# Performance work log

Measured on AMD Instinct MI355X. Metric: run time of the kernel, lower is better.

## Reference

```python
import jax, jax.numpy as jnp
import numpy as np

PAD = 0
N_SENSE = 5

def setup_inputs() -> dict:
    key = jax.random.key(0)
    k1, k2, k3, k4, k5 = jax.random.split(key, 5)
    mb, L, S, D, V, O = 256, 200, N_SENSE, 128, 50000, 50000
    inputs = jax.random.randint(k1, (mb, L * S), 0, V, dtype=jnp.int32).astype(jnp.int64)
    length_weights = jax.random.uniform(k2, (mb, 1, 1), dtype=jnp.float32)
    word_attn_mask = jnp.zeros((mb, L), dtype=bool)
    embedding = (jax.random.normal(k3, (V, D), dtype=jnp.float32) * 0.02).at[PAD].set(0.0)
    W_out = jax.random.normal(k4, (D, O), dtype=jnp.float32) * 0.02
    b_out = jnp.zeros((O,), dtype=jnp.float32)
    w_attn = jax.random.normal(k5, (D,), dtype=jnp.float32) * 0.02
    b_attn = jnp.zeros((), dtype=jnp.float32)
    return {"inputs": inputs, "length_weights": length_weights,
            "word_attn_mask": word_attn_mask, "embedding": embedding,
            "W_out": W_out, "b_out": b_out, "w_attn": w_attn, "b_attn": b_attn}

def reference(inputs, length_weights, word_attn_mask, embedding, W_out, b_out, w_attn, b_attn):
    S = N_SENSE
    mb, LS = inputs.shape
    L = LS // S
    D = embedding.shape[1]
    lw = length_weights[:, 0, 0]                      # [mb] per-example 1/length scalar
    embeds = embedding[inputs]                        # [mb, L*S, D]
    # global mean: sum over all sense-slots, scaled by length weight / n_sense
    gmean = embeds.sum(axis=1) * lw[:, None] / S      # [mb, D]
    # sense-level attention (softmax over n_sense per word slot)
    sense_imp = jnp.einsum('bld,bd->bl', embeds, gmean).reshape(mb, L, S)
    sense_w = jax.nn.softmax(sense_imp, axis=-1)      # [mb, L, S]
    word_mean = jnp.einsum('bls,blsd->bld', sense_w, embeds.reshape(mb, L, S, D))
    # word-level attention with pad mask
    word_imp = jnp.einsum('bld,d->bl', word_mean, w_attn) + b_attn
    word_imp = jnp.where(word_attn_mask, -jnp.inf, word_imp)
    word_w = jax.nn.softmax(word_imp, axis=-1)        # [mb, L]
    context = jnp.einsum('bl,bld->bd', word_w, word_mean)  # [mb, D]
    # similarity-based sense re-weighting
    sim = jnp.einsum('bld,bd->bl', embeds, context).reshape(mb, L, S)
    attn_w = jax.nn.softmax(sim, axis=-1).reshape(mb, LS)
    attn_w = attn_w * lw[:, None]
    attn_w = jnp.where(inputs == PAD, 0.0, attn_w)
    hidden = jnp.einsum('bl,bld->bd', attn_w, embeds)  # [mb, D]
    logits = hidden @ W_out + b_out
    return jax.nn.log_softmax(logits, axis=-1)
```

## Files before the change

### kernel.cpp

```cpp
#include <hip/hip_runtime.h>
#include <hip/hip_bf16.h>
#include <stdint.h>

#define MB 256
#define LW 200
#define NS 5
#define DD 128
#define OO 50000
#define LSTOK 1000

#define NSTRIPES 782
#define EMB_BLK 391

typedef __attribute__((ext_vector_type(8))) short bf16x8;
typedef __attribute__((ext_vector_type(4))) float f32x4;

__device__ inline unsigned short f2bf(float f){
  unsigned u = __float_as_uint(f);
  unsigned r = (u + 0x7fffu + ((u >> 16) & 1u)) >> 16;
  return (unsigned short)r;
}
__device__ inline float bf2f(unsigned short h){
  return __uint_as_float(((unsigned)h) << 16);
}
__device__ inline unsigned packbf(float a, float b){
  return (unsigned)f2bf(a) | ((unsigned)f2bf(b) << 16);
}
__device__ inline float lo16f(unsigned p){ return __uint_as_float(p << 16); }
__device__ inline float hi16f(unsigned p){ return __uint_as_float(p & 0xffff0000u); }
__device__ inline float wsum64(float v){
  #pragma unroll
  for (int o = 1; o < 64; o <<= 1) v += __shfl_xor(v, o, 64);
  return v;
}
__device__ inline float wmax64(float v){
  #pragma unroll
  for (int o = 1; o < 64; o <<= 1) v = fmaxf(v, __shfl_xor(v, o, 64));
  return v;
}
__device__ inline float dot8(uint4 r, float4 a, float4 b){
  return lo16f(r.x)*a.x + hi16f(r.x)*a.y + lo16f(r.y)*a.z + hi16f(r.y)*a.w
       + lo16f(r.z)*b.x + hi16f(r.z)*b.y + lo16f(r.w)*b.z + hi16f(r.w)*b.w;
}
__device__ inline void acc8(uint4 r, float4& x, float4& y){
  x.x += lo16f(r.x); x.y += hi16f(r.x); x.z += lo16f(r.y); x.w += hi16f(r.y);
  y.x += lo16f(r.z); y.y += hi16f(r.z); y.z += lo16f(r.w); y.w += hi16f(r.w);
}
__device__ inline void wacc8(uint4 r, float w, float4& x, float4& y){
  x.x += w*lo16f(r.x); x.y += w*hi16f(r.x); x.z += w*lo16f(r.y); x.w += w*hi16f(r.y);
  y.x += w*lo16f(r.z); y.y += w*hi16f(r.z); y.z += w*lo16f(r.w); y.w += w*hi16f(r.w);
}
__device__ inline float gsum16(float v){
  v += __shfl_xor(v, 1, 64);
  v += __shfl_xor(v, 2, 64);
  v += __shfl_xor(v, 4, 64);
  v += __shfl_xor(v, 8, 64);
  return v;
}
__device__ inline float xg(float v){
  v += __shfl_xor(v, 16, 64);
  v += __shfl_xor(v, 32, 64);
  return v;
}
__device__ inline int sniff_f(const unsigned* p, int l){
  unsigned v = p[2*l + 1];
  return (__ballot(v != 0u) == 0ull) ? 1 : 0;
}

__global__ __launch_bounds__(256) void k_prep(const float* __restrict__ W,
                                              const float* __restrict__ emb,
                                              unsigned short* __restrict__ Wt,
                                              unsigned* __restrict__ embB){
  int blk = blockIdx.x, t = threadIdx.x;
  if (blk < NSTRIPES){
    __shared__ float tile[64][129];
    long long n0 = (long long)blk * 64;
    int j = t & 63, kk = t >> 6;
    #pragma unroll
    for (int k = kk; k < 128; k += 4){
      float v = 0.f;
      if (n0 + j < OO) v = W[(long long)k*OO + n0 + j];
      tile[j][k] = v;
    }
    __syncthreads();
    #pragma unroll
    for (int c = t; c < 4096; c += 256){
      int row = c >> 6, dw = c & 63;
      if (n0 + row < OO){
        unsigned pr = packbf(tile[row][2*dw], tile[row][2*dw+1]);
        ((unsigned*)Wt)[(n0 + row)*64 + dw] = pr;
      }
    }
  } else {
    long long base = (long long)(blk - NSTRIPES) * 16384;
    for (int i = t; i < 4096; i += 256){
      long long idx = base + (long long)i*4;
      if (idx < (long long)OO*DD){
        float4 v = *(const float4*)(emb + idx);
        uint2 o; o.x = packbf(v.x, v.y); o.y = packbf(v.z, v.w);
        *(uint2*)(embB + (idx >> 1)) = o;
      }
    }
  }
}

__global__ __launch_bounds__(1024)
void k_attn(
    const int* __restrict__ in32, const float* __restrict__ lwp,
    const unsigned char* __restrict__ maskp, const unsigned* __restrict__ embB,
    const float* __restrict__ w_attn, const float* __restrict__ b_attn_p,
    unsigned short* __restrict__ hB)
{
  __shared__ float wm[LW*DD];
  __shared__ float red[16*DD];
  __shared__ int   idL[1024];
  __shared__ float gm[DD];
  __shared__ float cx[DD];
  __shared__ float waL[DD];
  __shared__ float wimp[LW];
  __shared__ float ww[LW];

  int b = blockIdx.x, t = threadIdx.x;
  int wv = t >> 6, l = t & 63;
  int g = l >> 4, q16 = l & 15;
  int G = wv*4 + g;
  int f = sniff_f((const unsigned*)in32, l);
  long long base = (long long)b * LSTOK;
  float lw = lwp[b];

  idL[t] = (t < LSTOK) ? in32[(base + t) << f] : 0;
  if (t < DD) waL[t] = w_attn[t];
  __syncthreads();

  {
    float4 s0v = {0,0,0,0}, s1v = {0,0,0,0};
    #pragma unroll 4
    for (int j = 0; j < 16; j++){
      int id = idL[G*16 + j];
      uint4 r = *(const uint4*)(embB + (long long)id*64 + (q16 << 2));
      acc8(r, s0v, s1v);
    }
    s0v.x = xg(s0v.x); s0v.y = xg(s0v.y); s0v.z = xg(s0v.z); s0v.w = xg(s0v.w);
    s1v.x = xg(s1v.x); s1v.y = xg(s1v.y); s1v.z = xg(s1v.z); s1v.w = xg(s1v.w);
    if (g == 0){
      *(float4*)&red[wv*DD + q16*8]     = s0v;
      *(float4*)&red[wv*DD + q16*8 + 4] = s1v;
    }
  }
  __syncthreads();
  if (t < DD){
    float s = 0.f;
    #pragma unroll
    for (int r = 0; r < 16; r++) s += red[r*DD + t];
    gm[t] = s * lw * 0.2f;
  }
  __syncthreads();

  {
    float4 g0v = *(const float4*)&gm[q16*8];
    float4 g1v = *(const float4*)&gm[q16*8+4];
    float4 wa0 = *(const float4*)&waL[q16*8];
    float4 wa1 = *(const float4*)&waL[q16*8+4];
    float b_attn = *b_attn_p;
    for (int w = G; w < LW; w += 64){
      int tb = w*NS;
      uint4 e0 = *(const uint4*)(embB + (long long)idL[tb  ]*64 + (q16<<2));
      uint4 e1 = *(const uint4*)(embB + (long long)idL[tb+1]*64 + (q16<<2));
      uint4 e2 = *(const uint4*)(embB + (long long)idL[tb+2]*64 + (q16<<2));
      uint4 e3 = *(const uint4*)(embB + (long long)idL[tb+3]*64 + (q16<<2));
      uint4 e4 = *(const uint4*)(embB + (long long)idL[tb+4]*64 + (q16<<2));
      float d0 = gsum16(dot8(e0, g0v, g1v));
      float d1 = gsum16(dot8(e1, g0v, g1v));
      float d2 = gsum16(dot8(e2, g0v, g1v));
      float d3 = gsum16(dot8(e3, g0v, g1v));
      float d4 = gsum16(dot8(e4, g0v, g1v));
      float mx = fmaxf(fmaxf(fmaxf(d0,d1), fmaxf(d2,d3)), d4);
      float x0 = __expf(d0-mx), x1 = __expf(d1-mx), x2 = __expf(d2-mx),
            x3 = __expf(d3-mx), x4 = __expf(d4-mx);
      float inv = 1.0f / (x0+x1+x2+x3+x4);
      float4 m0 = {0,0,0,0}, m1 = {0,0,0,0};
      wacc8(e0, x0*inv, m0, m1);
      wacc8(e1, x1*inv, m0, m1);
      wacc8(e2, x2*inv, m0, m1);
      wacc8(e3, x3*inv, m0, m1);
      wacc8(e4, x4*inv, m0, m1);
      *(float4*)&wm[w*DD + q16*8]     = m0;
      *(float4*)&wm[w*DD + q16*8 + 4] = m1;
      float wi = m0.x*wa0.x + m0.y*wa0.y + m0.z*wa0.z + m0.w*wa0.w
               + m1.x*wa1.x + m1.y*wa1.y + m1.z*wa1.z + m1.w*wa1.w;
      wi = gsum16(wi);
      if (q16 == 0)
        wimp[w] = maskp[(long long)b*LW + w] ? -INFINITY : (wi + b_attn);
    }
  }
  __syncthreads();

  if (wv == 0){
    float v[4]; float mx = -INFINITY;
    #pragma unroll
    for (int j = 0; j < 4; j++){
      int i = l + 64*j;
      v[j] = (i < LW) ? wimp[i] : -INFINITY;
      mx = fmaxf(mx, v[j]);
    }
    mx = wmax64(mx);
    float s = 0.f;
    #pragma unroll
    for (int j = 0; j < 4; j++){
      int i = l + 64*j;
      if (i < LW){ v[j] = __expf(v[j]-mx); s += v[j]; }
    }
    s = wsum64(s);
    float inv = 1.0f / s;
    #pragma unroll
    for (int j = 0; j < 4; j++){
      int i = l + 64*j;
      if (i < LW) ww[i] = v[j]*inv;
    }
  }
  __syncthreads();

  {
    int d = t & 127, r = t >> 7;
    float s = 0.f;
    for (int w = r; w < LW; w += 8) s += ww[w]*wm[w*DD + d];
    red[r*DD + d] = s;
  }
  __syncthreads();
  if (t < DD){
    float s = 0.f;
    #pragma unroll
    for (int r = 0; r < 8; r++) s += red[r*DD + t];
    cx[t] = s;
  }
  __syncthreads();

  {
    float4 c0v = *(const float4*)&cx[q16*8];
    float4 c1v = *(const float4*)&cx[q16*8+4];
    float4 h0a = {0,0,0,0}, h1a = {0,0,0,0};
    for (int w = G; w < LW; w += 64){
      int tb = w*NS;
      int i0 = idL[tb], i1 = idL[tb+1], i2 = idL[tb+2], i3 = idL[tb+3], i4 = idL[tb+4];
      uint4 e0 = *(const uint4*)(embB + (long long)i0*64 + (q16<<2));
      uint4 e1 = *(const uint4*)(embB + (long long)i1*64 + (q16<<2));
      uint4 e2 = *(const uint4*)(embB + (long long)i2*64 + (q16<<2));
      uint4 e3 = *(const uint4*)(embB + (long long)i3*64 + (q16<<2));
      uint4 e4 = *(const uint4*)(embB + (long long)i4*64 + (q16<<2));
      float d0 = gsum16(dot8(e0, c0v, c1v));
      float d1 = gsum16(dot8(e1, c0v, c1v));
      float d2 = gsum16(dot8(e2, c0v, c1v));
      float d3 = gsum16(dot8(e3, c0v, c1v));
      float d4 = gsum16(dot8(e4, c0v, c1v));
      float mx = fmaxf(fmaxf(fmaxf(d0,d1), fmaxf(d2,d3)), d4);
      float x0 = __expf(d0-mx), x1 = __expf(d1-mx), x2 = __expf(d2-mx),
            x3 = __expf(d3-mx), x4 = __expf(d4-mx);
      float inv = lw / (x0+x1+x2+x3+x4);
      wacc8(e0, (i0 == 0) ? 0.f : x0*inv, h0a, h1a);
      wacc8(e1, (i1 == 0) ? 0.f : x1*inv, h0a, h1a);
      wacc8(e2, (i2 == 0) ? 0.f : x2*inv, h0a, h1a);
      wacc8(e3, (i3 == 0) ? 0.f : x3*inv, h0a, h1a);
      wacc8(e4, (i4 == 0) ? 0.f : x4*inv, h0a, h1a);
    }
    h0a.x = xg(h0a.x); h0a.y = xg(h0a.y); h0a.z = xg(h0a.z); h0a.w = xg(h0a.w);
    h1a.x = xg(h1a.x); h1a.y = xg(h1a.y); h1a.z = xg(h1a.z); h1a.w = xg(h1a.w);
    if (g == 0){
      *(float4*)&red[wv*DD + q16*8]     = h0a;
      *(float4*)&red[wv*DD + q16*8 + 4] = h1a;
    }
  }
  __syncthreads();
  if (t < DD){
    float s = 0.f;
    #pragma unroll
    for (int r = 0; r < 16; r++) s += red[r*DD + t];
    hB[b*DD + t] = f2bf(s);
  }
}

__global__ __launch_bounds__(256) void k_gemm_stats(
    const unsigned short* __restrict__ Wt,
    const unsigned short* __restrict__ hB,
    const float* __restrict__ b_out,
    float* __restrict__ stats)
{
  __shared__ unsigned short Bs[64*128];
  int blk = blockIdx.x;
  long long n0 = (long long)blk * 64;
  int t = threadIdx.x;

  #pragma unroll
  for (int c = t; c < 1024; c += 256){
    int n = c >> 4;
    int bo = (c & 15) << 4;
    long long ng = n0 + n;
    uint4 v = {0u,0u,0u,0u};
    if (ng < OO) v = *(const uint4*)((const char*)Wt + ng*256 + bo);
    *(uint4*)((char*)Bs + n*256 + (bo ^ ((n & 7) << 4))) = v;
  }
  __syncthreads();

  int wv = t >> 6, l = t & 63;
  int lr = l & 15, lg = l >> 4;

  bf16x8 a[4][4];
  #pragma unroll
  for (int mt = 0; mt < 4; mt++)
    #pragma unroll
    for (int ks = 0; ks < 4; ks++)
      a[mt][ks] = *(const bf16x8*)(hB + (wv*64 + mt*16 + lr)*DD + ks*32 + lg*8);

  f32x4 acc[4][4];
  #pragma unroll
  for (int mt = 0; mt < 4; mt++)
    #pragma unroll
    for (int nt = 0; nt < 4; nt++)
      acc[mt][nt] = (f32x4){0.f,0.f,0.f,0.f};

  #pragma unroll
  for (int nt = 0; nt < 4; nt++)
    #pragma unroll
    for (int ks = 0; ks < 4; ks++){
      int n = nt*16 + lr;
      int kb = (ks*32 + lg*8) * 2;
      bf16x8 bfr = *(const bf16x8*)((const char*)Bs + n*256 + (kb ^ ((n & 7) << 4)));
      #pragma unroll
      for (int mt = 0; mt < 4; mt++)
        acc[mt][nt] = __builtin_amdgcn_mfma_f32_16x16x32_bf16(a[mt][ks], bfr, acc[mt][nt], 0, 0, 0);
    }

  float bv[4]; int nvalid[4];
  #pragma unroll
  for (int nt = 0; nt < 4; nt++){
    long long ng = n0 + nt*16 + lr;
    nvalid[nt] = (ng < OO);
    bv[nt] = nvalid[nt] ? b_out[ng] : 0.f;
  }
  #pragma unroll
  for (int mt = 0; mt < 4; mt++){
    #pragma unroll
    for (int j = 0; j < 4; j++){
      int m = wv*64 + mt*16 + lg*4 + j;
      float s = 0.f;
      #pragma unroll
      for (int nt = 0; nt < 4; nt++)
        s += nvalid[nt] ? __expf(acc[mt][nt][j] + bv[nt]) : 0.f;
      #pragma unroll
      for (int o = 1; o < 16; o <<= 1) s += __shfl_xor(s, o, 64);
      if (lr == 0) stats[(long long)m*NSTRIPES + blk] = s;
    }
  }
}

__global__ void k_reduce(const float* __restrict__ stats, float* __restrict__ Lrow){
  int m = blockIdx.x, l = threadIdx.x;
  float s = 0.f;
  for (int i = l; i < NSTRIPES; i += 64) s += stats[(long long)m*NSTRIPES + i];
  s = wsum64(s);
  if (l == 0) Lrow[m] = __logf(s);
}

__global__ __launch_bounds__(256) void k_gemm_out(
    const unsigned short* __restrict__ Wt,
    const unsigned short* __restrict__ hB,
    const float* __restrict__ b_out,
    const float* __restrict__ Lrow,
    float* __restrict__ out)
{
  __shared__ unsigned short Bs[64*128];
  int blk = blockIdx.x;
  long long n0 = (long long)blk * 64;
  int t = threadIdx.x;

  #pragma unroll
  for (int c = t; c < 1024; c += 256){
    int n = c >> 4;
    int bo = (c & 15) << 4;
    long long ng = n0 + n;
    uint4 v = {0u,0u,0u,0u};
    if (ng < OO) v = *(const uint4*)((const char*)Wt + ng*256 + bo);
    *(uint4*)((char*)Bs + n*256 + (bo ^ ((n & 7) << 4))) = v;
  }
  __syncthreads();

  int wv = t >> 6, l = t & 63;
  int lr = l & 15, lg = l >> 4;

  bf16x8 a[4][4];
  #pragma unroll
  for (int mt = 0; mt < 4; mt++)
    #pragma unroll
    for (int ks = 0; ks < 4; ks++)
      a[mt][ks] = *(const bf16x8*)(hB + (wv*64 + mt*16 + lr)*DD + ks*32 + lg*8);

  f32x4 acc[4][4];
  #pragma unroll
  for (int mt = 0; mt < 4; mt++)
    #pragma unroll
    for (int nt = 0; nt < 4; nt++)
      acc[mt][nt] = (f32x4){0.f,0.f,0.f,0.f};

  #pragma unroll
  for (int nt = 0; nt < 4; nt++)
    #pragma unroll
    for (int ks = 0; ks < 4; ks++){
      int n = nt*16 + lr;
      int kb = (ks*32 + lg*8) * 2;
      bf16x8 bfr = *(const bf16x8*)((const char*)Bs + n*256 + (kb ^ ((n & 7) << 4)));
      #pragma unroll
      for (int mt = 0; mt < 4; mt++)
        acc[mt][nt] = __builtin_amdgcn_mfma_f32_16x16x32_bf16(a[mt][ks], bfr, acc[mt][nt], 0, 0, 0);
    }

  float bv[4]; int nvalid[4]; long long ngl[4];
  #pragma unroll
  for (int nt = 0; nt < 4; nt++){
    long long ng = n0 + nt*16 + lr;
    ngl[nt] = ng;
    nvalid[nt] = (ng < OO);
    bv[nt] = nvalid[nt] ? b_out[ng] : 0.f;
  }
  #pragma unroll
  for (int mt = 0; mt < 4; mt++){
    #pragma unroll
    for (int j = 0; j < 4; j++){
      int m = wv*64 + mt*16 + lg*4 + j;
      float Lv = Lrow[m];
      #pragma unroll
      for (int nt = 0; nt < 4; nt++)
        if (nvalid[nt]) out[(long long)m*OO + ngl[nt]] = acc[mt][nt][j] + bv[nt] - Lv;
    }
  }
}

extern "C" void kernel_launch(void* const* d_in, const int* in_sizes, int n_in,
                              void* d_out, int out_size, void* d_ws, size_t ws_size,
                              hipStream_t stream)
{
  (void)in_sizes; (void)n_in; (void)out_size; (void)ws_size;
  const void* inputs          = d_in[0];
  const float* lw             = (const float*)d_in[1];
  const unsigned char* mask   = (const unsigned char*)d_in[2];
  const float* emb            = (const float*)d_in[3];
  const float* W              = (const float*)d_in[4];
  const float* bout           = (const float*)d_in[5];
  const float* w_attn         = (const float*)d_in[6];
  const float* b_attn         = (const float*)d_in[7];

  char* ws = (char*)d_ws;
  unsigned short* Wt   = (unsigned short*)(ws);
  unsigned* embB       = (unsigned*)(ws + 12800000);
  unsigned short* hB   = (unsigned short*)(ws + 25600000);
  float* stats         = (float*)(ws + 25665536);
  float* Lrow          = (float*)(ws + 26466304);

  const int* in32 = (const int*)inputs;

  k_prep<<<NSTRIPES + EMB_BLK, 256, 0, stream>>>(W, emb, Wt, embB);
  k_attn<<<MB, 1024, 0, stream>>>(in32, lw, mask, embB, w_attn, b_attn, hB);
  k_gemm_stats<<<NSTRIPES, 256, 0, stream>>>(Wt, hB, bout, stats);
  k_reduce<<<MB, 64, 0, stream>>>(stats, Lrow);
  k_gemm_out<<<NSTRIPES, 256, 0, stream>>>(Wt, hB, bout, Lrow, (float*)d_out);
}
```

Baseline: 99.71 us.

## Remap attention gathers to 32-lane word groups with two-word load batching

The attention kernel now assigns each word to a 32-lane group, with each lane loading 4 bf16 values (uint2) instead of 16-lane groups loading 8 (uint4). The gather loops are unrolled to issue the embedding loads for two words before computing on either, so more memory requests are in flight per wave. The aim is better latency hiding on the random embedding gathers and lower register pressure per lane. The cost is one more shuffle stage in each dot-product reduction and smaller per-lane loads.

Result: slower. 107.2 us (+7.5%).

```diff
diff --git a/kernel.cpp b/kernel.cpp
--- a/kernel.cpp
+++ b/kernel.cpp
@@ -38,33 +38,28 @@
   for (int o = 1; o < 64; o <<= 1) v = fmaxf(v, __shfl_xor(v, o, 64));
   return v;
 }
-__device__ inline float dot8(uint4 r, float4 a, float4 b){
-  return lo16f(r.x)*a.x + hi16f(r.x)*a.y + lo16f(r.y)*a.z + hi16f(r.y)*a.w
-       + lo16f(r.z)*b.x + hi16f(r.z)*b.y + lo16f(r.w)*b.z + hi16f(r.w)*b.w;
-}
-__device__ inline void acc8(uint4 r, float4& x, float4& y){
-  x.x += lo16f(r.x); x.y += hi16f(r.x); x.z += lo16f(r.y); x.w += hi16f(r.y);
-  y.x += lo16f(r.z); y.y += hi16f(r.z); y.z += lo16f(r.w); y.w += hi16f(r.w);
-}
-__device__ inline void wacc8(uint4 r, float w, float4& x, float4& y){
-  x.x += w*lo16f(r.x); x.y += w*hi16f(r.x); x.z += w*lo16f(r.y); x.w += w*hi16f(r.y);
-  y.x += w*lo16f(r.z); y.y += w*hi16f(r.z); y.z += w*lo16f(r.w); y.w += w*hi16f(r.w);
-}
-__device__ inline float gsum16(float v){
+__device__ inline float dot4u(uint2 r, float4 c){
+  return lo16f(r.x)*c.x + hi16f(r.x)*c.y + lo16f(r.y)*c.z + hi16f(r.y)*c.w;
+}
+__device__ inline float gsum32(float v){
   v += __shfl_xor(v, 1, 64);
   v += __shfl_xor(v, 2, 64);
   v += __shfl_xor(v, 4, 64);
   v += __shfl_xor(v, 8, 64);
-  return v;
-}
-__device__ inline float xg(float v){
   v += __shfl_xor(v, 16, 64);
-  v += __shfl_xor(v, 32, 64);
   return v;
 }
 __device__ inline int sniff_f(const unsigned* p, int l){
   unsigned v = p[2*l + 1];
   return (__ballot(v != 0u) == 0ull) ? 1 : 0;
+}
+
+struct W5 { uint2 e[5]; };
+__device__ inline void loadw(const unsigned* __restrict__ embB,
+                             const int* __restrict__ idL, int tb, int q, W5& w){
+  #pragma unroll
+  for (int s = 0; s < 5; s++)
+    w.e[s] = *(const uint2*)(embB + (long long)idL[tb + s]*64 + (q << 1));
 }
 
 __global__ __launch_bounds__(256) void k_prep(const float* __restrict__ W,
@@ -122,8 +117,8 @@
 
   int b = blockIdx.x, t = threadIdx.x;
   int wv = t >> 6, l = t & 63;
-  int g = l >> 4, q16 = l & 15;
-  int G = wv*4 + g;
+  int g2 = l >> 5, q = l & 31;
+  int G = wv*2 + g2;
   int f = sniff_f((const unsigned*)in32, l);
   long long base = (long long)b * LSTOK;
   float lw = lwp[b];
@@ -133,19 +128,17 @@
   __syncthreads();
 
   {
-    float4 s0v = {0,0,0,0}, s1v = {0,0,0,0};
+    float4 s = {0,0,0,0};
     #pragma unroll 4
-    for (int j = 0; j < 16; j++){
-      int id = idL[G*16 + j];
-      uint4 r = *(const uint4*)(embB + (long long)id*64 + (q16 << 2));
-      acc8(r, s0v, s1v);
-    }
-    s0v.x = xg(s0v.x); s0v.y = xg(s0v.y); s0v.z = xg(s0v.z); s0v.w = xg(s0v.w);
-    s1v.x = xg(s1v.x); s1v.y = xg(s1v.y); s1v.z = xg(s1v.z); s1v.w = xg(s1v.w);
-    if (g == 0){
-      *(float4*)&red[wv*DD + q16*8]     = s0v;
-      *(float4*)&red[wv*DD + q16*8 + 4] = s1v;
-    }
+    for (int j = 0; j < 32; j++){
+      int id = idL[G*32 + j];
+      uint2 r = *(const uint2*)(embB + (long long)id*64 + (q << 1));
+      s.x += lo16f(r.x); s.y += hi16f(r.x);
+      s.z += lo16f(r.y); s.w += hi16f(r.y);
+    }
+    s.x += __shfl_xor(s.x, 32, 64); s.y += __shfl_xor(s.y, 32, 64);
+    s.z += __shfl_xor(s.z, 32, 64); s.w += __shfl_xor(s.w, 32, 64);
+    if (g2 == 0) *(float4*)&red[wv*DD + q*4] = s;
   }
   __syncthreads();
   if (t < DD){
@@ -157,40 +150,48 @@
   __syncthreads();
 
   {
-    float4 g0v = *(const float4*)&gm[q16*8];
-    float4 g1v = *(const float4*)&gm[q16*8+4];
-    float4 wa0 = *(const float4*)&waL[q16*8];
-    float4 wa1 = *(const float4*)&waL[q16*8+4];
-    float b_attn = *b_attn_p;
-    for (int w = G; w < LW; w += 64){
-      int tb = w*NS;
-      uint4 e0 = *(const uint4*)(embB + (long long)idL[tb  ]*64 + (q16<<2));
-      uint4 e1 = *(const uint4*)(embB + (long long)idL[tb+1]*64 + (q16<<2));
-      uint4 e2 = *(const uint4*)(embB + (long long)idL[tb+2]*64 + (q16<<2));
-      uint4 e3 = *(const uint4*)(embB + (long long)idL[tb+3]*64 + (q16<<2));
-      uint4 e4 = *(const uint4*)(embB + (long long)idL[tb+4]*64 + (q16<<2));
-      float d0 = gsum16(dot8(e0, g0v, g1v));
-      float d1 = gsum16(dot8(e1, g0v, g1v));
-      float d2 = gsum16(dot8(e2, g0v, g1v));
-      float d3 = gsum16(dot8(e3, g0v, g1v));
-      float d4 = gsum16(dot8(e4, g0v, g1v));
+    float4 gv  = *(const float4*)&gm[q*4];
+    float4 wav = *(const float4*)&waL[q*4];
+    float ba = *b_attn_p;
+    const unsigned char* mrow = maskp + (long long)b*LW;
+
+    auto sense_word = [&](const W5& e, int wrd){
+      float d0 = gsum32(dot4u(e.e[0], gv));
+      float d1 = gsum32(dot4u(e.e[1], gv));
+      float d2 = gsum32(dot4u(e.e[2], gv));
+      float d3 = gsum32(dot4u(e.e[3], gv));
+      float d4 = gsum32(dot4u(e.e[4], gv));
       float mx = fmaxf(fmaxf(fmaxf(d0,d1), fmaxf(d2,d3)), d4);
       float x0 = __expf(d0-mx), x1 = __expf(d1-mx), x2 = __expf(d2-mx),
             x3 = __expf(d3-mx), x4 = __expf(d4-mx);
       float inv = 1.0f / (x0+x1+x2+x3+x4);
-      float4 m0 = {0,0,0,0}, m1 = {0,0,0,0};
-      wacc8(e0, x0*inv, m0, m1);
-      wacc8(e1, x1*inv, m0, m1);
-      wacc8(e2, x2*inv, m0, m1);
-      wacc8(e3, x3*inv, m0, m1);
-      wacc8(e4, x4*inv, m0, m1);
-      *(float4*)&wm[w*DD + q16*8]     = m0;
-      *(float4*)&wm[w*DD + q16*8 + 4] = m1;
-      float wi = m0.x*wa0.x + m0.y*wa0.y + m0.z*wa0.z + m0.w*wa0.w
-               + m1.x*wa1.x + m1.y*wa1.y + m1.z*wa1.z + m1.w*wa1.w;
-      wi = gsum16(wi);
-      if (q16 == 0)
-        wimp[w] = maskp[(long long)b*LW + w] ? -INFINITY : (wi + b_attn);
+      float4 m = {0,0,0,0};
+      float w0 = x0*inv, w1 = x1*inv, w2 = x2*inv, w3 = x3*inv, w4 = x4*inv;
+      m.x = w0*lo16f(e.e[0].x) + w1*lo16f(e.e[1].x) + w2*lo16f(e.e[2].x)
+          + w3*lo16f(e.e[3].x) + w4*lo16f(e.e[4].x);
+      m.y = w0*hi16f(e.e[0].x) + w1*hi16f(e.e[1].x) + w2*hi16f(e.e[2].x)
+          + w3*hi16f(e.e[3].x) + w4*hi16f(e.e[4].x);
+      m.z = w0*lo16f(e.e[0].y) + w1*lo16f(e.e[1].y) + w2*lo16f(e.e[2].y)
+          + w3*lo16f(e.e[3].y) + w4*lo16f(e.e[4].y);
+      m.w = w0*hi16f(e.e[0].y) + w1*hi16f(e.e[1].y) + w2*hi16f(e.e[2].y)
+          + w3*hi16f(e.e[3].y) + w4*hi16f(e.e[4].y);
+      *(float4*)&wm[wrd*DD + q*4] = m;
+      float wi = gsum32(m.x*wav.x + m.y*wav.y + m.z*wav.z + m.w*wav.w);
+      if (q == 0) wimp[wrd] = mrow[wrd] ? -INFINITY : (wi + ba);
+    };
+
+    for (int it = 0; it < 6; it += 2){
+      int wA = G + it*32, wB = wA + 32;
+      W5 eA, eB;
+      loadw(embB, idL, wA*NS, q, eA);
+      loadw(embB, idL, wB*NS, q, eB);
+      sense_word(eA, wA);
+      sense_word(eB, wB);
+    }
+    if (G < 8){
+      int wA = 192 + G;
+      W5 eA; loadw(embB, idL, wA*NS, q, eA);
+      sense_word(eA, wA);
     }
   }
   __syncthreads();
@@ -236,38 +237,51 @@
   __syncthreads();
 
   {
-    float4 c0v = *(const float4*)&cx[q16*8];
-    float4 c1v = *(const float4*)&cx[q16*8+4];
-    float4 h0a = {0,0,0,0}, h1a = {0,0,0,0};
-    for (int w = G; w < LW; w += 64){
-      int tb = w*NS;
-      int i0 = idL[tb], i1 = idL[tb+1], i2 = idL[tb+2], i3 = idL[tb+3], i4 = idL[tb+4];
-      uint4 e0 = *(const uint4*)(embB + (long long)i0*64 + (q16<<2));
-      uint4 e1 = *(const uint4*)(embB + (long long)i1*64 + (q16<<2));
-      uint4 e2 = *(const uint4*)(embB + (long long)i2*64 + (q16<<2));
-      uint4 e3 = *(const uint4*)(embB + (long long)i3*64 + (q16<<2));
-      uint4 e4 = *(const uint4*)(embB + (long long)i4*64 + (q16<<2));
-      float d0 = gsum16(dot8(e0, c0v, c1v));
-      float d1 = gsum16(dot8(e1, c0v, c1v));
-      float d2 = gsum16(dot8(e2, c0v, c1v));
-      float d3 = gsum16(dot8(e3, c0v, c1v));
-      float d4 = gsum16(dot8(e4, c0v, c1v));
+    float4 cv = *(const float4*)&cx[q*4];
+    float4 ha = {0,0,0,0};
+
+    auto sim_word = [&](const W5& e, int tb){
+      int i0 = idL[tb], i1 = idL[tb+1], i2 = idL[tb+2],
+          i3 = idL[tb+3], i4 = idL[tb+4];
+      float d0 = gsum32(dot4u(e.e[0], cv));
+      float d1 = gsum32(dot4u(e.e[1], cv));
+      float d2 = gsum32(dot4u(e.e[2], cv));
+      float d3 = gsum32(dot4u(e.e[3], cv));
+      float d4 = gsum32(dot4u(e.e[4], cv));
       float mx = fmaxf(fmaxf(fmaxf(d0,d1), fmaxf(d2,d3)), d4);
       float x0 = __expf(d0-mx), x1 = __expf(d1-mx), x2 = __expf(d2-mx),
             x3 = __expf(d3-mx), x4 = __expf(d4-mx);
       float inv = lw / (x0+x1+x2+x3+x4);
-      wacc8(e0, (i0 == 0) ? 0.f : x0*inv, h0a, h1a);
-      wacc8(e1, (i1 == 0) ? 0.f : x1*inv, h0a, h1a);
-      wacc8(e2, (i2 == 0) ? 0.f : x2*inv, h0a, h1a);
-      wacc8(e3, (i3 == 0) ? 0.f : x3*inv, h0a, h1a);
-      wacc8(e4, (i4 == 0) ? 0.f : x4*inv, h0a, h1a);
-    }
-    h0a.x = xg(h0a.x); h0a.y = xg(h0a.y); h0a.z = xg(h0a.z); h0a.w = xg(h0a.w);
-    h1a.x = xg(h1a.x); h1a.y = xg(h1a.y); h1a.z = xg(h1a.z); h1a.w = xg(h1a.w);
-    if (g == 0){
-      *(float4*)&red[wv*DD + q16*8]     = h0a;
-      *(float4*)&red[wv*DD + q16*8 + 4] = h1a;
-    }
+      float a0 = (i0==0)?0.f:x0*inv, a1 = (i1==0)?0.f:x1*inv,
+            a2 = (i2==0)?0.f:x2*inv, a3 = (i3==0)?0.f:x3*inv,
+            a4 = (i4==0)?0.f:x4*inv;
+      ha.x += a0*lo16f(e.e[0].x) + a1*lo16f(e.e[1].x) + a2*lo16f(e.e[2].x)
+            + a3*lo16f(e.e[3].x) + a4*lo16f(e.e[4].x);
+      ha.y += a0*hi16f(e.e[0].x) + a1*hi16f(e.e[1].x) + a2*hi16f(e.e[2].x)
+            + a3*hi16f(e.e[3].x) + a4*hi16f(e.e[4].x);
+      ha.z += a0*lo16f(e.e[0].y) + a1*lo16f(e.e[1].y) + a2*lo16f(e.e[2].y)
+            + a3*lo16f(e.e[3].y) + a4*lo16f(e.e[4].y);
+      ha.w += a0*hi16f(e.e[0].y) + a1*hi16f(e.e[1].y) + a2*hi16f(e.e[2].y)
+            + a3*hi16f(e.e[3].y) + a4*hi16f(e.e[4].y);
+    };
+
+    for (int it = 0; it < 6; it += 2){
+      int wA = G + it*32, wB = wA + 32;
+      W5 eA, eB;
+      loadw(embB, idL, wA*NS, q, eA);
+      loadw(embB, idL, wB*NS, q, eB);
+      sim_word(eA, wA*NS);
+      sim_word(eB, wB*NS);
+    }
+    if (G < 8){
+      int wA = 192 + G;
+      W5 eA; loadw(embB, idL, wA*NS, q, eA);
+      sim_word(eA, wA*NS);
+    }
+
+    ha.x += __shfl_xor(ha.x, 32, 64); ha.y += __shfl_xor(ha.y, 32, 64);
+    ha.z += __shfl_xor(ha.z, 32, 64); ha.w += __shfl_xor(ha.w, 32, 64);
+    if (g2 == 0) *(float4*)&red[wv*DD + q*4] = ha;
   }
   __syncthreads();
   if (t < DD){
```

## Store bf16 logits in stats GEMM and finalize with vectorized pass

Applied to the files above, without the earlier changes.

The stats GEMM now writes bias-added logits as bf16 to a workspace buffer while it accumulates exp sums. The second GEMM, which recomputed the same MFMA products, is replaced by a streaming kernel that reads the bf16 logits, subtracts the row log-sum-exp and writes fp32 output with 16-byte vector stores. This removes the duplicate W reload and matmul and replaces the old strided 4-byte output stores with coalesced ones. In exchange it adds about 25.6 MB of scattered 2-byte stores plus a 25.6 MB read-back, and rounds the logits to bf16 before normalisation.

Measured after the change: 102.1 us. 1.02x slower.

```diff
diff --git a/kernel.cpp b/kernel.cpp
--- a/kernel.cpp
+++ b/kernel.cpp
@@ -14,6 +14,7 @@
 
 typedef __attribute__((ext_vector_type(8))) short bf16x8;
 typedef __attribute__((ext_vector_type(4))) float f32x4;
+typedef __attribute__((ext_vector_type(8))) unsigned short u16x8;
 
 __device__ inline unsigned short f2bf(float f){
   unsigned u = __float_as_uint(f);
@@ -278,10 +279,11 @@
   }
 }
 
-__global__ __launch_bounds__(256) void k_gemm_stats(
+__global__ __launch_bounds__(256) void k_gemm(
     const unsigned short* __restrict__ Wt,
     const unsigned short* __restrict__ hB,
     const float* __restrict__ b_out,
+    unsigned short* __restrict__ logits,
     float* __restrict__ stats)
 {
   __shared__ unsigned short Bs[64*128];
@@ -329,10 +331,11 @@
         acc[mt][nt] = __builtin_amdgcn_mfma_f32_16x16x32_bf16(a[mt][ks], bfr, acc[mt][nt], 0, 0, 0);
     }
 
-  float bv[4]; int nvalid[4];
+  float bv[4]; int nvalid[4]; long long ngl[4];
   #pragma unroll
   for (int nt = 0; nt < 4; nt++){
     long long ng = n0 + nt*16 + lr;
+    ngl[nt] = ng;
     nvalid[nt] = (ng < OO);
     bv[nt] = nvalid[nt] ? b_out[ng] : 0.f;
   }
@@ -343,8 +346,13 @@
       int m = wv*64 + mt*16 + lg*4 + j;
       float s = 0.f;
       #pragma unroll
-      for (int nt = 0; nt < 4; nt++)
-        s += nvalid[nt] ? __expf(acc[mt][nt][j] + bv[nt]) : 0.f;
+      for (int nt = 0; nt < 4; nt++){
+        if (nvalid[nt]){
+          float x = acc[mt][nt][j] + bv[nt];
+          logits[(long long)m*OO + ngl[nt]] = f2bf(x);
+          s += __expf(x);
+        }
+      }
       #pragma unroll
       for (int o = 1; o < 16; o <<= 1) s += __shfl_xor(s, o, 64);
       if (lr == 0) stats[(long long)m*NSTRIPES + blk] = s;
@@ -360,77 +368,21 @@
   if (l == 0) Lrow[m] = __logf(s);
 }
 
-__global__ __launch_bounds__(256) void k_gemm_out(
-    const unsigned short* __restrict__ Wt,
-    const unsigned short* __restrict__ hB,
-    const float* __restrict__ b_out,
-    const float* __restrict__ Lrow,
-    float* __restrict__ out)
+__global__ __launch_bounds__(256) void k_finalize(
+    const unsigned short* __restrict__ logits,
+    const float* __restrict__ Lrow, float* __restrict__ out)
 {
-  __shared__ unsigned short Bs[64*128];
-  int blk = blockIdx.x;
-  long long n0 = (long long)blk * 64;
-  int t = threadIdx.x;
-
-  #pragma unroll
-  for (int c = t; c < 1024; c += 256){
-    int n = c >> 4;
-    int bo = (c & 15) << 4;
-    long long ng = n0 + n;
-    uint4 v = {0u,0u,0u,0u};
-    if (ng < OO) v = *(const uint4*)((const char*)Wt + ng*256 + bo);
-    *(uint4*)((char*)Bs + n*256 + (bo ^ ((n & 7) << 4))) = v;
-  }
-  __syncthreads();
-
-  int wv = t >> 6, l = t & 63;
-  int lr = l & 15, lg = l >> 4;
-
-  bf16x8 a[4][4];
-  #pragma unroll
-  for (int mt = 0; mt < 4; mt++)
-    #pragma unroll
-    for (int ks = 0; ks < 4; ks++)
-      a[mt][ks] = *(const bf16x8*)(hB + (wv*64 + mt*16 + lr)*DD + ks*32 + lg*8);
-
-  f32x4 acc[4][4];
-  #pragma unroll
-  for (int mt = 0; mt < 4; mt++)
-    #pragma unroll
-    for (int nt = 0; nt < 4; nt++)
-      acc[mt][nt] = (f32x4){0.f,0.f,0.f,0.f};
-
-  #pragma unroll
-  for (int nt = 0; nt < 4; nt++)
-    #pragma unroll
-    for (int ks = 0; ks < 4; ks++){
-      int n = nt*16 + lr;
-      int kb = (ks*32 + lg*8) * 2;
-      bf16x8 bfr = *(const bf16x8*)((const char*)Bs + n*256 + (kb ^ ((n & 7) << 4)));
-      #pragma unroll
-      for (int mt = 0; mt < 4; mt++)
-        acc[mt][nt] = __builtin_amdgcn_mfma_f32_16x16x32_bf16(a[mt][ks], bfr, acc[mt][nt], 0, 0, 0);
-    }
-
-  float bv[4]; int nvalid[4]; long long ngl[4];
-  #pragma unroll
-  for (int nt = 0; nt < 4; nt++){
-    long long ng = n0 + nt*16 + lr;
-    ngl[nt] = ng;
-    nvalid[nt] = (ng < OO);
-    bv[nt] = nvalid[nt] ? b_out[ng] : 0.f;
-  }
-  #pragma unroll
-  for (int mt = 0; mt < 4; mt++){
-    #pragma unroll
-    for (int j = 0; j < 4; j++){
-      int m = wv*64 + mt*16 + lg*4 + j;
-      float Lv = Lrow[m];
-      #pragma unroll
-      for (int nt = 0; nt < 4; nt++)
-        if (nvalid[nt]) out[(long long)m*OO + ngl[nt]] = acc[mt][nt][j] + bv[nt] - Lv;
-    }
-  }
+  long long c = (long long)blockIdx.x*256 + threadIdx.x;
+  int row = (int)(c / 6250);
+  float Lv = Lrow[row];
+  u16x8 v = *(const u16x8*)(logits + c*8);
+  float4 o0, o1;
+  o0.x = bf2f(v[0]) - Lv; o0.y = bf2f(v[1]) - Lv;
+  o0.z = bf2f(v[2]) - Lv; o0.w = bf2f(v[3]) - Lv;
+  o1.x = bf2f(v[4]) - Lv; o1.y = bf2f(v[5]) - Lv;
+  o1.z = bf2f(v[6]) - Lv; o1.w = bf2f(v[7]) - Lv;
+  *(float4*)(out + c*8)     = o0;
+  *(float4*)(out + c*8 + 4) = o1;
 }
 
 extern "C" void kernel_launch(void* const* d_in, const int* in_sizes, int n_in,
@@ -450,15 +402,16 @@
   char* ws = (char*)d_ws;
   unsigned short* Wt   = (unsigned short*)(ws);
   unsigned* embB       = (unsigned*)(ws + 12800000);
-  unsigned short* hB   = (unsigned short*)(ws + 25600000);
-  float* stats         = (float*)(ws + 25665536);
-  float* Lrow          = (float*)(ws + 26466304);
+  unsigned short* logits = (unsigned short*)(ws + 12800000);
+  unsigned short* hB   = (unsigned short*)(ws + 38400000);
+  float* stats         = (float*)(ws + 38465536);
+  float* Lrow          = (float*)(ws + 39266304);
 
   const int* in32 = (const int*)inputs;
 
   k_prep<<<NSTRIPES + EMB_BLK, 256, 0, stream>>>(W, emb, Wt, embB);
   k_attn<<<MB, 1024, 0, stream>>>(in32, lw, mask, embB, w_attn, b_attn, hB);
-  k_gemm_stats<<<NSTRIPES, 256, 0, stream>>>(Wt, hB, bout, stats);
+  k_gemm<<<NSTRIPES, 256, 0, stream>>>(Wt, hB, bout, logits, stats);
   k_reduce<<<MB, 64, 0, stream>>>(stats, Lrow);
-  k_gemm_out<<<NSTRIPES, 256, 0, stream>>>(Wt, hB, bout, Lrow, (float*)d_out);
-}
+  k_finalize<<<6250, 256, 0, stream>>>(logits, Lrow, (float*)d_out);
+}
```

## Fuse stats GEMM, reduce, and output GEMM into one cooperative kernel

Applied to the files above, without the earlier changes.

Replaces the three-kernel sequence (GEMM for exp-sum stats, per-row reduce, GEMM again for output) with a single cooperative kernel. It keeps the MFMA accumulators in registers across two grid-wide syncs, so the W tile is loaded and the GEMM computed only once. This also removes two kernel launches. In exchange it pays for two grid barriers, adds host-side attribute and occupancy queries on every call, and needs all 782 blocks co-resident, with a fallback to the old path if that fails.

New measurement: 100.0 us. No clear change (+0.3%).

```diff
diff --git a/kernel.cpp b/kernel.cpp
--- a/kernel.cpp
+++ b/kernel.cpp
@@ -1,6 +1,9 @@
 #include <hip/hip_runtime.h>
 #include <hip/hip_bf16.h>
+#include <hip/hip_cooperative_groups.h>
 #include <stdint.h>
+
+namespace cg = cooperative_groups;
 
 #define MB 256
 #define LW 200
@@ -19,9 +22,6 @@
   unsigned u = __float_as_uint(f);
   unsigned r = (u + 0x7fffu + ((u >> 16) & 1u)) >> 16;
   return (unsigned short)r;
-}
-__device__ inline float bf2f(unsigned short h){
-  return __uint_as_float(((unsigned)h) << 16);
 }
 __device__ inline unsigned packbf(float a, float b){
   return (unsigned)f2bf(a) | ((unsigned)f2bf(b) << 16);
@@ -278,64 +278,114 @@
   }
 }
 
+#define GEMM_BODY_STAGE_AND_MFMA()                                            \
+  __shared__ unsigned short Bs[64*128];                                       \
+  int blk = blockIdx.x;                                                       \
+  long long n0 = (long long)blk * 64;                                         \
+  int t = threadIdx.x;                                                        \
+  _Pragma("unroll")                                                           \
+  for (int c = t; c < 1024; c += 256){                                        \
+    int n = c >> 4;                                                           \
+    int bo = (c & 15) << 4;                                                   \
+    long long ng = n0 + n;                                                    \
+    uint4 v = {0u,0u,0u,0u};                                                  \
+    if (ng < OO) v = *(const uint4*)((const char*)Wt + ng*256 + bo);          \
+    *(uint4*)((char*)Bs + n*256 + (bo ^ ((n & 7) << 4))) = v;                 \
+  }                                                                           \
+  __syncthreads();                                                            \
+  int wv = t >> 6, l = t & 63;                                                \
+  int lr = l & 15, lg = l >> 4;                                               \
+  bf16x8 a[4][4];                                                             \
+  _Pragma("unroll")                                                           \
+  for (int mt = 0; mt < 4; mt++)                                              \
+    _Pragma("unroll")                                                         \
+    for (int ks = 0; ks < 4; ks++)                                            \
+      a[mt][ks] = *(const bf16x8*)(hB + (wv*64 + mt*16 + lr)*DD + ks*32 + lg*8); \
+  f32x4 acc[4][4];                                                            \
+  _Pragma("unroll")                                                           \
+  for (int mt = 0; mt < 4; mt++)                                              \
+    _Pragma("unroll")                                                         \
+    for (int nt = 0; nt < 4; nt++)                                            \
+      acc[mt][nt] = (f32x4){0.f,0.f,0.f,0.f};                                 \
+  _Pragma("unroll")                                                           \
+  for (int nt = 0; nt < 4; nt++)                                              \
+    _Pragma("unroll")                                                         \
+    for (int ks = 0; ks < 4; ks++){                                           \
+      int n = nt*16 + lr;                                                     \
+      int kb = (ks*32 + lg*8) * 2;                                            \
+      bf16x8 bfr = *(const bf16x8*)((const char*)Bs + n*256 + (kb ^ ((n & 7) << 4))); \
+      _Pragma("unroll")                                                       \
+      for (int mt = 0; mt < 4; mt++)                                          \
+        acc[mt][nt] = __builtin_amdgcn_mfma_f32_16x16x32_bf16(a[mt][ks], bfr, acc[mt][nt], 0, 0, 0); \
+    }                                                                         \
+  float bv[4]; int nvalid[4]; long long ngl[4];                               \
+  _Pragma("unroll")                                                           \
+  for (int nt = 0; nt < 4; nt++){                                             \
+    long long ng = n0 + nt*16 + lr;                                           \
+    ngl[nt] = ng;                                                             \
+    nvalid[nt] = (ng < OO);                                                   \
+    bv[nt] = nvalid[nt] ? b_out[ng] : 0.f;                                    \
+  }
+
+__global__ __launch_bounds__(256) void k_gemm_fused(
+    const unsigned short* __restrict__ Wt,
+    const unsigned short* __restrict__ hB,
+    const float* __restrict__ b_out,
+    float* __restrict__ stats,
+    float* __restrict__ Lrow,
+    float* __restrict__ out)
+{
+  GEMM_BODY_STAGE_AND_MFMA()
+
+  #pragma unroll
+  for (int mt = 0; mt < 4; mt++){
+    #pragma unroll
+    for (int j = 0; j < 4; j++){
+      int m = wv*64 + mt*16 + lg*4 + j;
+      float s = 0.f;
+      #pragma unroll
+      for (int nt = 0; nt < 4; nt++)
+        s += nvalid[nt] ? __expf(acc[mt][nt][j] + bv[nt]) : 0.f;
+      #pragma unroll
+      for (int o = 1; o < 16; o <<= 1) s += __shfl_xor(s, o, 64);
+      if (lr == 0) stats[(long long)m*NSTRIPES + blk] = s;
+    }
+  }
+
+  __threadfence();
+  cg::this_grid().sync();
+
+  if (blk < MB && wv == 0){
+    float s = 0.f;
+    for (int i = l; i < NSTRIPES; i += 64)
+      s += stats[(long long)blk*NSTRIPES + i];
+    s = wsum64(s);
+    if (l == 0) Lrow[blk] = __logf(s);
+  }
+
+  __threadfence();
+  cg::this_grid().sync();
+
+  #pragma unroll
+  for (int mt = 0; mt < 4; mt++){
+    #pragma unroll
+    for (int j = 0; j < 4; j++){
+      int m = wv*64 + mt*16 + lg*4 + j;
+      float Lv = Lrow[m];
+      #pragma unroll
+      for (int nt = 0; nt < 4; nt++)
+        if (nvalid[nt]) out[(long long)m*OO + ngl[nt]] = acc[mt][nt][j] + bv[nt] - Lv;
+    }
+  }
+}
+
 __global__ __launch_bounds__(256) void k_gemm_stats(
     const unsigned short* __restrict__ Wt,
     const unsigned short* __restrict__ hB,
     const float* __restrict__ b_out,
     float* __restrict__ stats)
 {
-  __shared__ unsigned short Bs[64*128];
-  int blk = blockIdx.x;
-  long long n0 = (long long)blk * 64;
-  int t = threadIdx.x;
-
-  #pragma unroll
-  for (int c = t; c < 1024; c += 256){
-    int n = c >> 4;
-    int bo = (c & 15) << 4;
-    long long ng = n0 + n;
-    uint4 v = {0u,0u,0u,0u};
-    if (ng < OO) v = *(const uint4*)((const char*)Wt + ng*256 + bo);
-    *(uint4*)((char*)Bs + n*256 + (bo ^ ((n & 7) << 4))) = v;
-  }
-  __syncthreads();
-
-  int wv = t >> 6, l = t & 63;
-  int lr = l & 15, lg = l >> 4;
-
-  bf16x8 a[4][4];
-  #pragma unroll
-  for (int mt = 0; mt < 4; mt++)
-    #pragma unroll
-    for (int ks = 0; ks < 4; ks++)
-      a[mt][ks] = *(const bf16x8*)(hB + (wv*64 + mt*16 + lr)*DD + ks*32 + lg*8);
-
-  f32x4 acc[4][4];
-  #pragma unroll
-  for (int mt = 0; mt < 4; mt++)
-    #pragma unroll
-    for (int nt = 0; nt < 4; nt++)
-      acc[mt][nt] = (f32x4){0.f,0.f,0.f,0.f};
-
-  #pragma unroll
-  for (int nt = 0; nt < 4; nt++)
-    #pragma unroll
-    for (int ks = 0; ks < 4; ks++){
-      int n = nt*16 + lr;
-      int kb = (ks*32 + lg*8) * 2;
-      bf16x8 bfr = *(const bf16x8*)((const char*)Bs + n*256 + (kb ^ ((n & 7) << 4)));
-      #pragma unroll
-      for (int mt = 0; mt < 4; mt++)
-        acc[mt][nt] = __builtin_amdgcn_mfma_f32_16x16x32_bf16(a[mt][ks], bfr, acc[mt][nt], 0, 0, 0);
-    }
-
-  float bv[4]; int nvalid[4];
-  #pragma unroll
-  for (int nt = 0; nt < 4; nt++){
-    long long ng = n0 + nt*16 + lr;
-    nvalid[nt] = (ng < OO);
-    bv[nt] = nvalid[nt] ? b_out[ng] : 0.f;
-  }
+  GEMM_BODY_STAGE_AND_MFMA()
   #pragma unroll
   for (int mt = 0; mt < 4; mt++){
     #pragma unroll
@@ -350,6 +400,7 @@
       if (lr == 0) stats[(long long)m*NSTRIPES + blk] = s;
     }
   }
+  (void)ngl;
 }
 
 __global__ void k_reduce(const float* __restrict__ stats, float* __restrict__ Lrow){
@@ -367,59 +418,7 @@
     const float* __restrict__ Lrow,
     float* __restrict__ out)
 {
-  __shared__ unsigned short Bs[64*128];
-  int blk = blockIdx.x;
-  long long n0 = (long long)blk * 64;
-  int t = threadIdx.x;
-
-  #pragma unroll
-  for (int c = t; c < 1024; c += 256){
-    int n = c >> 4;
-    int bo = (c & 15) << 4;
-    long long ng = n0 + n;
-    uint4 v = {0u,0u,0u,0u};
-    if (ng < OO) v = *(const uint4*)((const char*)Wt + ng*256 + bo);
-    *(uint4*)((char*)Bs + n*256 + (bo ^ ((n & 7) << 4))) = v;
-  }
-  __syncthreads();
-
-  int wv = t >> 6, l = t & 63;
-  int lr = l & 15, lg = l >> 4;
-
-  bf16x8 a[4][4];
-  #pragma unroll
-  for (int mt = 0; mt < 4; mt++)
-    #pragma unroll
-    for (int ks = 0; ks < 4; ks++)
-      a[mt][ks] = *(const bf16x8*)(hB + (wv*64 + mt*16 + lr)*DD + ks*32 + lg*8);
-
-  f32x4 acc[4][4];
-  #pragma unroll
-  for (int mt = 0; mt < 4; mt++)
-    #pragma unroll
-    for (int nt = 0; nt < 4; nt++)
-      acc[mt][nt] = (f32x4){0.f,0.f,0.f,0.f};
-
-  #pragma unroll
-  for (int nt = 0; nt < 4; nt++)
-    #pragma unroll
-    for (int ks = 0; ks < 4; ks++){
-      int n = nt*16 + lr;
-      int kb = (ks*32 + lg*8) * 2;
-      bf16x8 bfr = *(const bf16x8*)((const char*)Bs + n*256 + (kb ^ ((n & 7) << 4)));
-      #pragma unroll
-      for (int mt = 0; mt < 4; mt++)
-        acc[mt][nt] = __builtin_amdgcn_mfma_f32_16x16x32_bf16(a[mt][ks], bfr, acc[mt][nt], 0, 0, 0);
-    }
-
-  float bv[4]; int nvalid[4]; long long ngl[4];
-  #pragma unroll
-  for (int nt = 0; nt < 4; nt++){
-    long long ng = n0 + nt*16 + lr;
-    ngl[nt] = ng;
-    nvalid[nt] = (ng < OO);
-    bv[nt] = nvalid[nt] ? b_out[ng] : 0.f;
-  }
+  GEMM_BODY_STAGE_AND_MFMA()
   #pragma unroll
   for (int mt = 0; mt < 4; mt++){
     #pragma unroll
@@ -455,10 +454,36 @@
   float* Lrow          = (float*)(ws + 26466304);
 
   const int* in32 = (const int*)inputs;
+  float* outp = (float*)d_out;
 
   k_prep<<<NSTRIPES + EMB_BLK, 256, 0, stream>>>(W, emb, Wt, embB);
   k_attn<<<MB, 1024, 0, stream>>>(in32, lw, mask, embB, w_attn, b_attn, hB);
-  k_gemm_stats<<<NSTRIPES, 256, 0, stream>>>(Wt, hB, bout, stats);
-  k_reduce<<<MB, 64, 0, stream>>>(stats, Lrow);
-  k_gemm_out<<<NSTRIPES, 256, 0, stream>>>(Wt, hB, bout, Lrow, (float*)d_out);
-}
+
+  int dev = 0;
+  hipGetDevice(&dev);
+  int coopAttr = 0, nCU = 0, maxBlkPerCU = 0;
+  hipDeviceGetAttribute(&coopAttr, hipDeviceAttributeCooperativeLaunch, dev);
+  hipDeviceGetAttribute(&nCU, hipDeviceAttributeMultiprocessorCount, dev);
+  hipOccupancyMaxActiveBlocksPerMultiprocessor(&maxBlkPerCU, k_gemm_fused, 256, 0);
+
+  bool useCoop = (coopAttr != 0) && ((long long)maxBlkPerCU * nCU >= NSTRIPES);
+  if (useCoop){
+    const unsigned short* aWt = Wt;
+    const unsigned short* ahB = hB;
+    const float* ab = bout;
+    float* ast = stats;
+    float* aL = Lrow;
+    float* ao = outp;
+    void* ka[] = {(void*)&aWt, (void*)&ahB, (void*)&ab,
+                  (void*)&ast, (void*)&aL, (void*)&ao};
+    hipError_t e = hipLaunchCooperativeKernel((const void*)k_gemm_fused,
+                                              dim3(NSTRIPES), dim3(256),
+                                              ka, 0, stream);
+    if (e != hipSuccess) useCoop = false;
+  }
+  if (!useCoop){
+    k_gemm_stats<<<NSTRIPES, 256, 0, stream>>>(Wt, hB, bout, stats);
+    k_reduce<<<MB, 64, 0, stream>>>(stats, Lrow);
+    k_gemm_out<<<NSTRIPES, 256, 0, stream>>>(Wt, hB, bout, Lrow, outp);
+  }
+}
```
